# Optimization experiments

Measured on AMD Instinct MI355X. Metric: run time of the kernel, lower is better.

## Reference

```python
import jax, jax.numpy as jnp
import numpy as np

B, N, OBS, H, A = 1024, 64, 128, 256, 16
NH = 4
HD = H // NH


def _linear_params(key, fan_in, fan_out):
    k1, k2 = jax.random.split(key)
    bound = 1.0 / np.sqrt(fan_in)
    W = jax.random.uniform(k1, (fan_out, fan_in), jnp.float32, -bound, bound)
    b = jax.random.uniform(k2, (fan_out,), jnp.float32, -bound, bound)
    return W, b


def setup_inputs() -> dict:
    key = jax.random.key(0)
    ks = jax.random.split(key, 10)
    obs = jax.random.normal(ks[0], (B, N, OBS), jnp.float32)
    adj = jax.random.randint(ks[1], (B, N, N), 0, 2).astype(jnp.float32)
    # guarantee every row has at least one neighbor (self-loop) so softmax is finite
    adj = jnp.maximum(adj, jnp.eye(N, dtype=jnp.float32)[None])
    W1, b1 = _linear_params(ks[2], OBS, H)
    W2, b2 = _linear_params(ks[3], H, H)
    Wq, bq = _linear_params(ks[4], H, H)
    Wk, bk = _linear_params(ks[5], H, H)
    Wv, bv = _linear_params(ks[6], H, H)
    Wo, bo = _linear_params(ks[7], H, H)
    Wc, bc = _linear_params(ks[8], H, H)
    W3, b3 = _linear_params(ks[9], H, A)
    return dict(obs=obs, adj=adj, W1=W1, b1=b1, W2=W2, b2=b2,
                Wq=Wq, bq=bq, Wk=Wk, bk=bk, Wv=Wv, bv=bv,
                Wo=Wo, bo=bo, Wc=Wc, bc=bc, W3=W3, b3=b3)


def reference(obs, adj, W1, b1, W2, b2, Wq, bq, Wk, bk, Wv, bv, Wo, bo, Wc, bc, W3, b3):
    lin = lambda x, W, b: jnp.einsum('bnd,od->bno', x, W) + b
    x = jax.nn.relu(lin(obs, W1, b1))
    x = jax.nn.relu(lin(x, W2, b2))
    # multi-head attention with adjacency mask
    def heads(t):  # [B,N,H] -> [B,NH,N,HD]
        return t.reshape(B, N, NH, HD).transpose(0, 2, 1, 3)
    q = heads(lin(x, Wq, bq))
    k = heads(lin(x, Wk, bk))
    v = heads(lin(x, Wv, bv))
    scores = jnp.einsum('bhqd,bhkd->bhqk', q, k) / np.sqrt(HD).astype(np.float32)
    scores = jnp.where(adj[:, None] == 0, -jnp.inf, scores)
    attn = jax.nn.softmax(scores, axis=-1)
    out = jnp.einsum('bhqk,bhkd->bhqd', attn, v)
    out = out.transpose(0, 2, 1, 3).reshape(B, N, H)
    x = lin(out, Wo, bo)
    # communication: adj @ fc(x)
    x = jnp.einsum('bnm,bmh->bnh', adj, lin(x, Wc, bc))
    return lin(x, W3, b3)
```

## Files before the change

### kernel.cpp

```cpp
#include <hip/hip_runtime.h>
#include <stdint.h>

typedef unsigned short u16;
typedef unsigned long long u64;
typedef __attribute__((ext_vector_type(8))) short short8;
typedef __attribute__((ext_vector_type(4))) float f32x4;

#define MFMA16 __builtin_amdgcn_mfma_f32_16x16x32_bf16

#define B_ 1024
#define N_ 64
#define MTOT (B_ * N_)

__device__ __forceinline__ u16 f2bf(float f) {
  union { float f; uint32_t u; } v; v.f = f;
  uint32_t r = v.u + 0x7FFFu + ((v.u >> 16) & 1u);
  return (u16)(r >> 16);
}

union U8 { short8 v; u16 u[8]; };
union U4 { u64 v; u16 u[4]; };

__device__ __forceinline__ void cp16(const void* g, void* l) {
  __builtin_amdgcn_global_load_lds(
      (const __attribute__((address_space(1))) void*)g,
      (__attribute__((address_space(3))) void*)l, 16, 0, 0);
}

__global__ __launch_bounds__(256) void k_l1(
    const float* __restrict__ obs, u16* __restrict__ obsb,
    const float* __restrict__ Wc, const float* __restrict__ Wo,
    const float* __restrict__ bo, const float* __restrict__ bc,
    float* __restrict__ M1, float* __restrict__ bv,
    const float* __restrict__ W1, const float* __restrict__ W2,
    const float* __restrict__ Wq, const float* __restrict__ Wk,
    u16* o1, u16* o2, u16* oq, u16* ok) {
  const int bid = blockIdx.x, tid = threadIdx.x;
  if (bid < 4096) {
    const int e = (bid * 256 + tid) * 8;
    f32x4 a = *(const f32x4*)(obs + e);
    f32x4 b = *(const f32x4*)(obs + e + 4);
    U8 pk;
#pragma unroll
    for (int j = 0; j < 4; j++) { pk.u[j] = f2bf(a[j]); pk.u[4 + j] = f2bf(b[j]); }
    *(short8*)(obsb + e) = pk.v;
  } else if (bid < 4352) {
    __shared__ float wcr[256];
    __shared__ float red[4];
    const int j = bid - 4096, d = tid;
    wcr[d] = Wc[j * 256 + d];
    __syncthreads();
    float acc = 0.f;
    for (int i = 0; i < 256; i++) acc += wcr[i] * Wo[i * 256 + d];
    M1[j * 256 + d] = acc;
    float p = wcr[d] * bo[d];
    for (int off = 32; off >= 1; off >>= 1) p += __shfl_xor(p, off);
    if ((d & 63) == 0) red[d >> 6] = p;
    __syncthreads();
    if (d == 0) bv[j] = bc[j] + red[0] + red[1] + red[2] + red[3];
  } else {
    int off8 = (bid - 4352) * 256 + tid;
    const float* src; u16* dst;
    if      (off8 <  4096) { src = W1; dst = o1; }
    else if (off8 < 12288) { src = W2; dst = o2; off8 -= 4096; }
    else if (off8 < 20480) { src = Wq; dst = oq; off8 -= 12288; }
    else                   { src = Wk; dst = ok; off8 -= 20480; }
    const int e = off8 * 8;
    f32x4 a = *(const f32x4*)(src + e);
    f32x4 b = *(const f32x4*)(src + e + 4);
    U8 pk;
#pragma unroll
    for (int j = 0; j < 4; j++) { pk.u[j] = f2bf(a[j]); pk.u[4 + j] = f2bf(b[j]); }
    *(short8*)(dst + e) = pk.v;
  }
}

template<int K>
__device__ __forceinline__ void gemm_full(
    const u16* __restrict__ A, const u16* __restrict__ W,
    const float* __restrict__ bias, u16* __restrict__ C,
    const int m0, const bool relu, char* smem) {
  char* As  = smem;
  char* Bs0 = smem + 16384;
  char* Bs1 = smem + 32768;
  const int tid = threadIdx.x;
  const int lane = tid & 63, wid = tid >> 6;
  const int wr = wid >> 1, wc = wid & 1;
  const int ro = lane & 15, hi = lane >> 4;

  f32x4 acc0[4][4], acc1[4][4];
#pragma unroll
  for (int m = 0; m < 4; m++)
#pragma unroll
    for (int n = 0; n < 4; n++) {
      acc0[m][n] = (f32x4){0.f, 0.f, 0.f, 0.f};
      acc1[m][n] = (f32x4){0.f, 0.f, 0.f, 0.f};
    }

  for (int k0 = 0; k0 < K; k0 += 64) {
#pragma unroll
    for (int i = 0; i < 4; i++) {
      const int boff = i * 4096 + wid * 1024;
      const int t = boff + lane * 16;
      const int row = t >> 7;
      const int cb = (t & 127) ^ ((row & 7) << 4);
      cp16(A + (size_t)(m0 + row) * K + k0 + (cb >> 1), As + boff);
      cp16(W + (size_t)row * K + k0 + (cb >> 1), Bs0 + boff);
      cp16(W + (size_t)(128 + row) * K + k0 + (cb >> 1), Bs1 + boff);
    }
    __syncthreads();
#pragma unroll
    for (int kk = 0; kk < 64; kk += 32) {
      short8 af[4], b0[4], b1[4];
#pragma unroll
      for (int m = 0; m < 4; m++) {
        const int row = wr * 64 + m * 16 + ro;
        af[m] = *(const short8*)(As + ((row * 128 + (kk + hi * 8) * 2) ^ ((row & 7) << 4)));
      }
#pragma unroll
      for (int n = 0; n < 4; n++) {
        const int row = wc * 64 + n * 16 + ro;
        const int off = (row * 128 + (kk + hi * 8) * 2) ^ ((row & 7) << 4);
        b0[n] = *(const short8*)(Bs0 + off);
        b1[n] = *(const short8*)(Bs1 + off);
      }
#pragma unroll
      for (int m = 0; m < 4; m++)
#pragma unroll
        for (int n = 0; n < 4; n++) {
          acc0[m][n] = MFMA16(af[m], b0[n], acc0[m][n], 0, 0, 0);
          acc1[m][n] = MFMA16(af[m], b1[n], acc1[m][n], 0, 0, 0);
        }
    }
    __syncthreads();
  }

  u16 (*Cs)[136] = (u16(*)[136])smem;
  auto ep = [&](f32x4 (&acc)[4][4], const int n0) {
#pragma unroll
    for (int half = 0; half < 2; half++) {
      if (wr == half) {
#pragma unroll
        for (int n = 0; n < 4; n++) {
          const int col = wc * 64 + n * 16 + ro;
          const float bb = bias[n0 + col];
#pragma unroll
          for (int m = 0; m < 4; m++)
#pragma unroll
            for (int j = 0; j < 4; j++) {
              float val = acc[m][n][j] + bb;
              if (relu) val = fmaxf(val, 0.f);
              Cs[m * 16 + hi * 4 + j][col] = f2bf(val);
            }
        }
      }
      __syncthreads();
      for (int i = tid; i < 64 * 16; i += 256) {
        const int r = i >> 4, c = (i & 15) << 3;
        *(short8*)(C + (size_t)(m0 + half * 64 + r) * 256 + n0 + c) = *(short8*)&Cs[r][c];
      }
      __syncthreads();
    }
  };
  ep(acc0, 0);
  ep(acc1, 128);
}

__global__ __launch_bounds__(256, 2) void k_gemm1_prep2(
    const u16* __restrict__ obsb, const u16* __restrict__ W1b,
    const float* __restrict__ b1, u16* __restrict__ x1,
    const float* __restrict__ W3, const float* __restrict__ M1,
    const float* __restrict__ bvchain, const float* __restrict__ bvw,
    float* __restrict__ Wzf, float* __restrict__ bz) {
  __shared__ char smem[49152];
  if (blockIdx.x < 512) {
    gemm_full<128>(obsb, W1b, b1, x1, (int)blockIdx.x * 128, true, smem);
    return;
  }
  float* w3r = (float*)smem;
  float* red = (float*)(smem + 1024);
  const int a = blockIdx.x - 512, d = threadIdx.x;
  w3r[d] = W3[a * 256 + d];
  __syncthreads();
  float acc = 0.f;
  for (int j = 0; j < 256; j++) acc += w3r[j] * M1[j * 256 + d];
  Wzf[a * 256 + d] = acc;
  float p = w3r[d] * bvchain[d] + acc * bvw[d];
  for (int off = 32; off >= 1; off >>= 1) p += __shfl_xor(p, off);
  if ((d & 63) == 0) red[d >> 6] = p;
  __syncthreads();
  if (d == 0) bz[a] = red[0] + red[1] + red[2] + red[3];
}

__global__ __launch_bounds__(256, 2) void k_x2_prep3(
    const u16* __restrict__ x1, const u16* __restrict__ W2b,
    const float* __restrict__ b2, u16* __restrict__ x2,
    const float* __restrict__ Wzf, const float* __restrict__ Wv,
    u16* __restrict__ G) {
  __shared__ char smem[49152];
  if (blockIdx.x < 512) {
    gemm_full<256>(x1, W2b, b2, x2, (int)blockIdx.x * 128, true, smem);
    return;
  }
  const int g = blockIdx.x - 512, d2 = threadIdx.x;
  const int h = g >> 4, a = g & 15;
  float* wzr = (float*)smem;
  if (d2 < 64) wzr[d2] = Wzf[a * 256 + h * 64 + d2];
  __syncthreads();
  float acc = 0.f;
#pragma unroll 8
  for (int d = 0; d < 64; d++) acc += wzr[d] * Wv[(size_t)(h * 64 + d) * 256 + d2];
  G[g * 256 + d2] = f2bf(acc);
}

__global__ __launch_bounds__(256, 2) void k_qk_gemmv(
    const u16* __restrict__ x2,
    const u16* __restrict__ Wqb, const float* __restrict__ bq, u16* __restrict__ Qg,
    const u16* __restrict__ Wkb, const float* __restrict__ bk, u16* __restrict__ Kg,
    const u16* __restrict__ G, u16* __restrict__ Vzt) {
  __shared__ char smem[49152];
  const int bid = blockIdx.x;
  if (bid < 1024) {
    const int q = bid >> 4, r = bid & 15;
    const int mt = q * 8 + (r & 7);
    const int sub = r >> 3;
    gemm_full<256>(x2, sub ? Wkb : Wqb, sub ? bk : bq, sub ? Kg : Qg,
                   mt * 128, false, smem);
    return;
  }
  char* As = smem;
  char* Bs = smem + 16384;
  const int tid = threadIdx.x;
  const int lane = tid & 63, w = tid >> 6;
  const int ro = lane & 15, hi = lane >> 4;
  const int m0 = (bid - 1024) * 128;

  f32x4 acc[2][4];
#pragma unroll
  for (int m = 0; m < 2; m++)
#pragma unroll
    for (int n = 0; n < 4; n++) acc[m][n] = (f32x4){0.f, 0.f, 0.f, 0.f};

  for (int k0 = 0; k0 < 256; k0 += 64) {
#pragma unroll
    for (int i = 0; i < 4; i++) {
      const int boff = i * 4096 + w * 1024;
      const int t = boff + lane * 16;
      const int row = t >> 7;
      const int cb = (t & 127) ^ ((row & 7) << 4);
      cp16(x2 + (size_t)(m0 + row) * 256 + k0 + (cb >> 1), As + boff);
    }
    {
      const int boff = w * 1024;
      const int t = boff + lane * 16;
      const int row = t >> 7;
      const int cb = (t & 127) ^ ((row & 7) << 4);
      cp16(G + (size_t)row * 256 + k0 + (cb >> 1), Bs + boff);
      const int boff2 = 4096 + w * 1024;
      const int t2 = boff2 + lane * 16;
      const int row2 = t2 >> 7;
      const int cb2 = (t2 & 127) ^ ((row2 & 7) << 4);
      cp16(G + (size_t)row2 * 256 + k0 + (cb2 >> 1), Bs + boff2);
    }
    __syncthreads();
#pragma unroll
    for (int kk = 0; kk < 64; kk += 32) {
      short8 af[2], bfr[4];
#pragma unroll
      for (int m = 0; m < 2; m++) {
        const int row = w * 32 + m * 16 + ro;
        af[m] = *(const short8*)(As + ((row * 128 + (kk + hi * 8) * 2) ^ ((row & 7) << 4)));
      }
#pragma unroll
      for (int n = 0; n < 4; n++) {
        const int row = n * 16 + ro;
        bfr[n] = *(const short8*)(Bs + ((row * 128 + (kk + hi * 8) * 2) ^ ((row & 7) << 4)));
      }
#pragma unroll
      for (int m = 0; m < 2; m++)
#pragma unroll
        for (int n = 0; n < 4; n++)
          acc[m][n] = MFMA16(af[m], bfr[n], acc[m][n], 0, 0, 0);
    }
    __syncthreads();
  }

#pragma unroll
  for (int m = 0; m < 2; m++) {
    const int rbase = w * 32 + m * 16;
    const int bidx = (m0 >> 6) + (rbase >> 6);
    const int ke = (rbase + hi * 4) & 63;
#pragma unroll
    for (int n = 0; n < 4; n++) {
      const int c = n * 16 + ro;
      U4 pk;
#pragma unroll
      for (int j = 0; j < 4; j++) pk.u[j] = f2bf(acc[m][n][j]);
      *(u64*)(Vzt + (size_t)bidx * 4096 + (size_t)c * 64 + ke) = pk.v;
    }
  }
}

__global__ __launch_bounds__(256, 2) void attn_fused(
    const u16* __restrict__ Qg, const u16* __restrict__ Kg,
    const u16* __restrict__ Vzt, const float* __restrict__ adj,
    const float* __restrict__ bz, const float* __restrict__ b3,
    float* __restrict__ out) {
  __shared__ u16 Ps[4][64][72];
  __shared__ float Zs[4][64][16];
  __shared__ u64 adjm[64];
  __shared__ u16 chunk[64][4];

  const int b = blockIdx.x, tid = threadIdx.x;
  const int lane = tid & 63, w = tid >> 6;
  const int ro = lane & 15, hi = lane >> 4;
  const int hc = w * 64;
  const size_t base = (size_t)b * 64 * 256;

  short8 kb[4][2];
#pragma unroll
  for (int n = 0; n < 4; n++)
#pragma unroll
    for (int ks = 0; ks < 2; ks++)
      kb[n][ks] = *(const short8*)(Kg + base + (size_t)(n * 16 + ro) * 256 + hc + ks * 32 + hi * 8);

  {
    const int q = tid >> 2, qa = tid & 3;
    const float* ar = adj + ((size_t)b * 64 + q) * 64 + qa * 16;
    f32x4 a0 = *(const f32x4*)(ar);
    f32x4 a1 = *(const f32x4*)(ar + 4);
    f32x4 a2 = *(const f32x4*)(ar + 8);
    f32x4 a3 = *(const f32x4*)(ar + 12);
    unsigned m16 = 0;
#pragma unroll
    for (int i = 0; i < 4; i++) {
      m16 |= (unsigned)(a0[i] != 0.f) << i;
      m16 |= (unsigned)(a1[i] != 0.f) << (4 + i);
      m16 |= (unsigned)(a2[i] != 0.f) << (8 + i);
      m16 |= (unsigned)(a3[i] != 0.f) << (12 + i);
    }
    chunk[q][qa] = (u16)m16;
  }

  f32x4 s[4][4];
#pragma unroll
  for (int m = 0; m < 4; m++) {
    short8 af[2];
#pragma unroll
    for (int ks = 0; ks < 2; ks++)
      af[ks] = *(const short8*)(Qg + base + (size_t)(m * 16 + ro) * 256 + hc + ks * 32 + hi * 8);
#pragma unroll
    for (int n = 0; n < 4; n++) s[m][n] = (f32x4){0.f, 0.f, 0.f, 0.f};
#pragma unroll
    for (int ks = 0; ks < 2; ks++)
#pragma unroll
      for (int n = 0; n < 4; n++)
        s[m][n] = MFMA16(af[ks], kb[n][ks], s[m][n], 0, 0, 0);
  }

  short8 vz[2];
#pragma unroll
  for (int ks = 0; ks < 2; ks++)
    vz[ks] = *(const short8*)(Vzt + (size_t)b * 4096 + (size_t)(hc / 4 + ro) * 64 + ks * 32 + hi * 8);

  __syncthreads();
  if (tid < 64)
    adjm[tid] = (u64)chunk[tid][0] | ((u64)chunk[tid][1] << 16) |
                ((u64)chunk[tid][2] << 32) | ((u64)chunk[tid][3] << 48);
  __syncthreads();

#pragma unroll
  for (int m = 0; m < 4; m++) {
#pragma unroll
    for (int j = 0; j < 4; j++) {
      const int q = m * 16 + hi * 4 + j;
      const u64 msk = adjm[q];
      float sv[4], ev[4];
      float mx = -3.0e38f;
#pragma unroll
      for (int n = 0; n < 4; n++) {
        const bool on = (msk >> (n * 16 + ro)) & 1ull;
        sv[n] = on ? s[m][n][j] * 0.125f : -3.0e38f;
        mx = fmaxf(mx, sv[n]);
      }
      mx = fmaxf(mx, __shfl_xor(mx, 1));
      mx = fmaxf(mx, __shfl_xor(mx, 2));
      mx = fmaxf(mx, __shfl_xor(mx, 4));
      mx = fmaxf(mx, __shfl_xor(mx, 8));
      float sum = 0.f;
#pragma unroll
      for (int n = 0; n < 4; n++) {
        ev[n] = (sv[n] > -1.0e37f) ? __expf(sv[n] - mx) : 0.f;
        sum += ev[n];
      }
      sum += __shfl_xor(sum, 1);
      sum += __shfl_xor(sum, 2);
      sum += __shfl_xor(sum, 4);
      sum += __shfl_xor(sum, 8);
      const float inv = 1.0f / sum;
#pragma unroll
      for (int n = 0; n < 4; n++)
        Ps[w][q][n * 16 + ro] = f2bf(ev[n] * inv);
    }
  }

#pragma unroll
  for (int m = 0; m < 4; m++) {
    short8 pa[2];
    pa[0] = *(const short8*)&Ps[w][m * 16 + ro][hi * 8];
    pa[1] = *(const short8*)&Ps[w][m * 16 + ro][32 + hi * 8];
    f32x4 oz = (f32x4){0.f, 0.f, 0.f, 0.f};
#pragma unroll
    for (int ks = 0; ks < 2; ks++)
      oz = MFMA16(pa[ks], vz[ks], oz, 0, 0, 0);
#pragma unroll
    for (int j = 0; j < 4; j++)
      Zs[w][m * 16 + hi * 4 + j][ro] = oz[j];
  }
  __syncthreads();

  for (int i = tid; i < 1024; i += 256) {
    const int r = i >> 4, a = i & 15;
    Zs[0][r][a] += Zs[1][r][a] + Zs[2][r][a] + Zs[3][r][a];
  }
  __syncthreads();

  {
    const int n = tid >> 2, a4 = (tid & 3) << 2;
    const u64 msk = adjm[n];
    const float deg = (float)__popcll(msk);
    float a0 = 0.f, a1 = 0.f, a2 = 0.f, a3 = 0.f;
#pragma unroll 8
    for (int m = 0; m < 64; m++) {
      const float wv = (float)((msk >> m) & 1ull);
      f32x4 z = *(const f32x4*)&Zs[0][m][a4];
      a0 += wv * z[0]; a1 += wv * z[1]; a2 += wv * z[2]; a3 += wv * z[3];
    }
    f32x4 r;
    r[0] = a0 + b3[a4 + 0] + deg * bz[a4 + 0];
    r[1] = a1 + b3[a4 + 1] + deg * bz[a4 + 1];
    r[2] = a2 + b3[a4 + 2] + deg * bz[a4 + 2];
    r[3] = a3 + b3[a4 + 3] + deg * bz[a4 + 3];
    *(f32x4*)(out + ((size_t)b * 64 + n) * 16 + a4) = r;
  }
}

extern "C" void kernel_launch(void* const* d_in, const int* in_sizes, int n_in,
                              void* d_out, int out_size, void* d_ws, size_t ws_size,
                              hipStream_t stream) {
  const float* obs = (const float*)d_in[0];
  const float* adj = (const float*)d_in[1];
  const float* W1  = (const float*)d_in[2];
  const float* b1  = (const float*)d_in[3];
  const float* W2  = (const float*)d_in[4];
  const float* b2  = (const float*)d_in[5];
  const float* Wq  = (const float*)d_in[6];
  const float* bq  = (const float*)d_in[7];
  const float* Wk  = (const float*)d_in[8];
  const float* bk  = (const float*)d_in[9];
  const float* Wv  = (const float*)d_in[10];
  const float* bvw = (const float*)d_in[11];
  const float* Wo  = (const float*)d_in[12];
  const float* bo  = (const float*)d_in[13];
  const float* Wc  = (const float*)d_in[14];
  const float* bc  = (const float*)d_in[15];
  const float* W3  = (const float*)d_in[16];
  const float* b3  = (const float*)d_in[17];
  float* out = (float*)d_out;

  char* ws = (char*)d_ws;
  const size_t BIG = (size_t)MTOT * 256 * 2;
  u16* buf0 = (u16*)(ws);
  u16* buf1 = (u16*)(ws + BIG);
  u16* buf2 = (u16*)(ws + 2 * BIG);
  u16* buf3 = (u16*)(ws + 3 * BIG);
  char* p = ws + 4 * BIG;
  u16* W1b = (u16*)p;              p += 128 * 256 * 2;
  u16* W2b = (u16*)p;              p += 256 * 256 * 2;
  u16* Wqb = (u16*)p;              p += 256 * 256 * 2;
  u16* Wkb = (u16*)p;              p += 256 * 256 * 2;
  float* M1 = (float*)p;           p += 256 * 256 * 4;
  float* Wzf = (float*)p;          p += 16 * 256 * 4;
  u16* G   = (u16*)p;              p += 64 * 256 * 2;
  float* bv = (float*)p;           p += 256 * 4;
  float* bz = (float*)p;           p += 16 * 4;
  u16* obsb = (u16*)p;             p += (size_t)MTOT * 128 * 2;

  dim3 blk(256);
  k_l1<<<dim3(4464), blk, 0, stream>>>(obs, obsb, Wc, Wo, bo, bc, M1, bv,
                                       W1, W2, Wq, Wk, W1b, W2b, Wqb, Wkb);
  k_gemm1_prep2<<<dim3(528), blk, 0, stream>>>(obsb, W1b, b1, buf0,
                                               W3, M1, bv, bvw, Wzf, bz);
  k_x2_prep3<<<dim3(576), blk, 0, stream>>>(buf0, W2b, b2, buf1, Wzf, Wv, G);
  k_qk_gemmv<<<dim3(1536), blk, 0, stream>>>(buf1, Wqb, bq, buf2,
                                             Wkb, bk, buf3, G, buf0);
  attn_fused<<<dim3(1024), blk, 0, stream>>>(buf2, buf3, buf0, adj, bz, b3, out);
}
```

Baseline: 125.2 us.

## Double-buffer GEMM K-loop and fuse obs bf16 conversion into first GEMM

```diff
diff --git a/kernel.cpp b/kernel.cpp
--- a/kernel.cpp
+++ b/kernel.cpp
@@ -8,9 +8,7 @@
 
 #define MFMA16 __builtin_amdgcn_mfma_f32_16x16x32_bf16
 
-#define B_ 1024
-#define N_ 64
-#define MTOT (B_ * N_)
+#define MTOT 65536
 
 __device__ __forceinline__ u16 f2bf(float f) {
   union { float f; uint32_t u; } v; v.f = f;
@@ -28,7 +26,6 @@
 }
 
 __global__ __launch_bounds__(256) void k_l1(
-    const float* __restrict__ obs, u16* __restrict__ obsb,
     const float* __restrict__ Wc, const float* __restrict__ Wo,
     const float* __restrict__ bo, const float* __restrict__ bc,
     float* __restrict__ M1, float* __restrict__ bv,
@@ -36,18 +33,10 @@
     const float* __restrict__ Wq, const float* __restrict__ Wk,
     u16* o1, u16* o2, u16* oq, u16* ok) {
   const int bid = blockIdx.x, tid = threadIdx.x;
-  if (bid < 4096) {
-    const int e = (bid * 256 + tid) * 8;
-    f32x4 a = *(const f32x4*)(obs + e);
-    f32x4 b = *(const f32x4*)(obs + e + 4);
-    U8 pk;
-#pragma unroll
-    for (int j = 0; j < 4; j++) { pk.u[j] = f2bf(a[j]); pk.u[4 + j] = f2bf(b[j]); }
-    *(short8*)(obsb + e) = pk.v;
-  } else if (bid < 4352) {
+  if (bid < 256) {
     __shared__ float wcr[256];
     __shared__ float red[4];
-    const int j = bid - 4096, d = tid;
+    const int j = bid, d = tid;
     wcr[d] = Wc[j * 256 + d];
     __syncthreads();
     float acc = 0.f;
@@ -59,7 +48,7 @@
     __syncthreads();
     if (d == 0) bv[j] = bc[j] + red[0] + red[1] + red[2] + red[3];
   } else {
-    int off8 = (bid - 4352) * 256 + tid;
+    int off8 = (bid - 256) * 256 + tid;
     const float* src; u16* dst;
     if      (off8 <  4096) { src = W1; dst = o1; }
     else if (off8 < 12288) { src = W2; dst = o2; off8 -= 4096; }
@@ -75,14 +64,11 @@
   }
 }
 
-template<int K>
-__device__ __forceinline__ void gemm_full(
-    const u16* __restrict__ A, const u16* __restrict__ W,
+template<int K, bool AF32>
+__device__ __forceinline__ void gemm_full2(
+    const void* __restrict__ Ain, const u16* __restrict__ W,
     const float* __restrict__ bias, u16* __restrict__ C,
     const int m0, const bool relu, char* smem) {
-  char* As  = smem;
-  char* Bs0 = smem + 16384;
-  char* Bs1 = smem + 32768;
   const int tid = threadIdx.x;
   const int lane = tid & 63, wid = tid >> 6;
   const int wr = wid >> 1, wc = wid & 1;
@@ -97,43 +83,81 @@
       acc1[m][n] = (f32x4){0.f, 0.f, 0.f, 0.f};
     }
 
-  for (int k0 = 0; k0 < K; k0 += 64) {
+  auto stage = [&](int buf, int k0) {
+    char* Ax = smem + buf * 24576;
+    char* Bx = Ax + 8192;
+    if (AF32) {
+      const float* Af = (const float*)Ain;
+#pragma unroll
+      for (int it = 0; it < 2; it++) {
+        const int e = (tid + it * 256) * 8;
+        const int r = e >> 5, c = e & 31;
+        const float* s = Af + (size_t)(m0 + r) * K + k0 + c;
+        f32x4 a = *(const f32x4*)s, b = *(const f32x4*)(s + 4);
+        U8 pk;
+#pragma unroll
+        for (int j = 0; j < 4; j++) { pk.u[j] = f2bf(a[j]); pk.u[4 + j] = f2bf(b[j]); }
+        *(short8*)(Ax + ((r * 64 + c * 2) ^ ((r & 3) << 4))) = pk.v;
+      }
+    } else {
+      const u16* Ab = (const u16*)Ain;
+#pragma unroll
+      for (int i = 0; i < 2; i++) {
+        const int boff = i * 4096 + wid * 1024;
+        const int t = boff + lane * 16;
+        const int row = t >> 6;
+        const int cb = (t & 63) ^ ((row & 3) << 4);
+        cp16(Ab + (size_t)(m0 + row) * K + k0 + (cb >> 1), Ax + boff);
+      }
+    }
 #pragma unroll
     for (int i = 0; i < 4; i++) {
       const int boff = i * 4096 + wid * 1024;
       const int t = boff + lane * 16;
-      const int row = t >> 7;
-      const int cb = (t & 127) ^ ((row & 7) << 4);
-      cp16(A + (size_t)(m0 + row) * K + k0 + (cb >> 1), As + boff);
-      cp16(W + (size_t)row * K + k0 + (cb >> 1), Bs0 + boff);
-      cp16(W + (size_t)(128 + row) * K + k0 + (cb >> 1), Bs1 + boff);
-    }
+      const int row = t >> 6;
+      const int cb = (t & 63) ^ ((row & 3) << 4);
+      cp16(W + (size_t)row * K + k0 + (cb >> 1), Bx + boff);
+    }
+  };
+
+  auto compute = [&](int buf) {
+    char* Ax = smem + buf * 24576;
+    char* Bx = Ax + 8192;
+    short8 af[4], fb0[4], fb1[4];
+#pragma unroll
+    for (int m = 0; m < 4; m++) {
+      const int row = wr * 64 + m * 16 + ro;
+      af[m] = *(const short8*)(Ax + ((row * 64 + hi * 16) ^ ((row & 3) << 4)));
+    }
+#pragma unroll
+    for (int n = 0; n < 4; n++) {
+      const int r0 = wc * 64 + n * 16 + ro;
+      fb0[n] = *(const short8*)(Bx + ((r0 * 64 + hi * 16) ^ ((r0 & 3) << 4)));
+      const int r1 = 128 + r0;
+      fb1[n] = *(const short8*)(Bx + ((r1 * 64 + hi * 16) ^ ((r1 & 3) << 4)));
+    }
+    __builtin_amdgcn_s_setprio(1);
+#pragma unroll
+    for (int m = 0; m < 4; m++)
+#pragma unroll
+      for (int n = 0; n < 4; n++) {
+        acc0[m][n] = MFMA16(af[m], fb0[n], acc0[m][n], 0, 0, 0);
+        acc1[m][n] = MFMA16(af[m], fb1[n], acc1[m][n], 0, 0, 0);
+      }
+    __builtin_amdgcn_s_setprio(0);
+  };
+
+  stage(0, 0);
+  __syncthreads();
+  int cur = 0;
+  for (int k0 = 32; k0 < K; k0 += 32) {
+    stage(cur ^ 1, k0);
+    compute(cur);
     __syncthreads();
-#pragma unroll
-    for (int kk = 0; kk < 64; kk += 32) {
-      short8 af[4], b0[4], b1[4];
-#pragma unroll
-      for (int m = 0; m < 4; m++) {
-        const int row = wr * 64 + m * 16 + ro;
-        af[m] = *(const short8*)(As + ((row * 128 + (kk + hi * 8) * 2) ^ ((row & 7) << 4)));
-      }
-#pragma unroll
-      for (int n = 0; n < 4; n++) {
-        const int row = wc * 64 + n * 16 + ro;
-        const int off = (row * 128 + (kk + hi * 8) * 2) ^ ((row & 7) << 4);
-        b0[n] = *(const short8*)(Bs0 + off);
-        b1[n] = *(const short8*)(Bs1 + off);
-      }
-#pragma unroll
-      for (int m = 0; m < 4; m++)
-#pragma unroll
-        for (int n = 0; n < 4; n++) {
-          acc0[m][n] = MFMA16(af[m], b0[n], acc0[m][n], 0, 0, 0);
-          acc1[m][n] = MFMA16(af[m], b1[n], acc1[m][n], 0, 0, 0);
-        }
-    }
-    __syncthreads();
-  }
+    cur ^= 1;
+  }
+  compute(cur);
+  __syncthreads();
 
   u16 (*Cs)[136] = (u16(*)[136])smem;
   auto ep = [&](f32x4 (&acc)[4][4], const int n0) {
@@ -167,14 +191,14 @@
 }
 
 __global__ __launch_bounds__(256, 2) void k_gemm1_prep2(
-    const u16* __restrict__ obsb, const u16* __restrict__ W1b,
+    const float* __restrict__ obs, const u16* __restrict__ W1b,
     const float* __restrict__ b1, u16* __restrict__ x1,
     const float* __restrict__ W3, const float* __restrict__ M1,
     const float* __restrict__ bvchain, const float* __restrict__ bvw,
     float* __restrict__ Wzf, float* __restrict__ bz) {
   __shared__ char smem[49152];
   if (blockIdx.x < 512) {
-    gemm_full<128>(obsb, W1b, b1, x1, (int)blockIdx.x * 128, true, smem);
+    gemm_full2<128, true>(obs, W1b, b1, x1, (int)blockIdx.x * 128, true, smem);
     return;
   }
   float* w3r = (float*)smem;
@@ -199,7 +223,7 @@
     u16* __restrict__ G) {
   __shared__ char smem[49152];
   if (blockIdx.x < 512) {
-    gemm_full<256>(x1, W2b, b2, x2, (int)blockIdx.x * 128, true, smem);
+    gemm_full2<256, false>(x1, W2b, b2, x2, (int)blockIdx.x * 128, true, smem);
     return;
   }
   const int g = blockIdx.x - 512, d2 = threadIdx.x;
@@ -224,12 +248,10 @@
     const int q = bid >> 4, r = bid & 15;
     const int mt = q * 8 + (r & 7);
     const int sub = r >> 3;
-    gemm_full<256>(x2, sub ? Wkb : Wqb, sub ? bk : bq, sub ? Kg : Qg,
-                   mt * 128, false, smem);
+    gemm_full2<256, false>(x2, sub ? Wkb : Wqb, sub ? bk : bq, sub ? Kg : Qg,
+                           mt * 128, false, smem);
     return;
   }
-  char* As = smem;
-  char* Bs = smem + 16384;
   const int tid = threadIdx.x;
   const int lane = tid & 63, w = tid >> 6;
   const int ro = lane & 15, hi = lane >> 4;
@@ -241,49 +263,58 @@
 #pragma unroll
     for (int n = 0; n < 4; n++) acc[m][n] = (f32x4){0.f, 0.f, 0.f, 0.f};
 
-  for (int k0 = 0; k0 < 256; k0 += 64) {
-#pragma unroll
-    for (int i = 0; i < 4; i++) {
+  auto stage = [&](int buf, int k0) {
+    char* Ax = smem + buf * 12288;
+    char* Bx = Ax + 8192;
+#pragma unroll
+    for (int i = 0; i < 2; i++) {
       const int boff = i * 4096 + w * 1024;
       const int t = boff + lane * 16;
-      const int row = t >> 7;
-      const int cb = (t & 127) ^ ((row & 7) << 4);
-      cp16(x2 + (size_t)(m0 + row) * 256 + k0 + (cb >> 1), As + boff);
+      const int row = t >> 6;
+      const int cb = (t & 63) ^ ((row & 3) << 4);
+      cp16(x2 + (size_t)(m0 + row) * 256 + k0 + (cb >> 1), Ax + boff);
     }
     {
       const int boff = w * 1024;
       const int t = boff + lane * 16;
-      const int row = t >> 7;
-      const int cb = (t & 127) ^ ((row & 7) << 4);
-      cp16(G + (size_t)row * 256 + k0 + (cb >> 1), Bs + boff);
-      const int boff2 = 4096 + w * 1024;
-      const int t2 = boff2 + lane * 16;
-      const int row2 = t2 >> 7;
-      const int cb2 = (t2 & 127) ^ ((row2 & 7) << 4);
-      cp16(G + (size_t)row2 * 256 + k0 + (cb2 >> 1), Bs + boff2);
-    }
+      const int row = t >> 6;
+      const int cb = (t & 63) ^ ((row & 3) << 4);
+      cp16(G + (size_t)row * 256 + k0 + (cb >> 1), Bx + boff);
+    }
+  };
+  auto compute = [&](int buf) {
+    char* Ax = smem + buf * 12288;
+    char* Bx = Ax + 8192;
+    short8 af[2], fb[4];
+#pragma unroll
+    for (int m = 0; m < 2; m++) {
+      const int row = w * 32 + m * 16 + ro;
+      af[m] = *(const short8*)(Ax + ((row * 64 + hi * 16) ^ ((row & 3) << 4)));
+    }
+#pragma unroll
+    for (int n = 0; n < 4; n++) {
+      const int row = n * 16 + ro;
+      fb[n] = *(const short8*)(Bx + ((row * 64 + hi * 16) ^ ((row & 3) << 4)));
+    }
+    __builtin_amdgcn_s_setprio(1);
+#pragma unroll
+    for (int m = 0; m < 2; m++)
+#pragma unroll
+      for (int n = 0; n < 4; n++)
+        acc[m][n] = MFMA16(af[m], fb[n], acc[m][n], 0, 0, 0);
+    __builtin_amdgcn_s_setprio(0);
+  };
+
+  stage(0, 0);
+  __syncthreads();
+  int cur = 0;
+  for (int k0 = 32; k0 < 256; k0 += 32) {
+    stage(cur ^ 1, k0);
+    compute(cur);
     __syncthreads();
-#pragma unroll
-    for (int kk = 0; kk < 64; kk += 32) {
-      short8 af[2], bfr[4];
-#pragma unroll
-      for (int m = 0; m < 2; m++) {
-        const int row = w * 32 + m * 16 + ro;
-        af[m] = *(const short8*)(As + ((row * 128 + (kk + hi * 8) * 2) ^ ((row & 7) << 4)));
-      }
-#pragma unroll
-      for (int n = 0; n < 4; n++) {
-        const int row = n * 16 + ro;
-        bfr[n] = *(const short8*)(Bs + ((row * 128 + (kk + hi * 8) * 2) ^ ((row & 7) << 4)));
-      }
-#pragma unroll
-      for (int m = 0; m < 2; m++)
-#pragma unroll
-        for (int n = 0; n < 4; n++)
-          acc[m][n] = MFMA16(af[m], bfr[n], acc[m][n], 0, 0, 0);
-    }
-    __syncthreads();
-  }
+    cur ^= 1;
+  }
+  compute(cur);
 
 #pragma unroll
   for (int m = 0; m < 2; m++) {
@@ -484,12 +515,11 @@
   u16* G   = (u16*)p;              p += 64 * 256 * 2;
   float* bv = (float*)p;           p += 256 * 4;
   float* bz = (float*)p;           p += 16 * 4;
-  u16* obsb = (u16*)p;             p += (size_t)MTOT * 128 * 2;
 
   dim3 blk(256);
-  k_l1<<<dim3(4464), blk, 0, stream>>>(obs, obsb, Wc, Wo, bo, bc, M1, bv,
-                                       W1, W2, Wq, Wk, W1b, W2b, Wqb, Wkb);
-  k_gemm1_prep2<<<dim3(528), blk, 0, stream>>>(obsb, W1b, b1, buf0,
+  k_l1<<<dim3(368), blk, 0, stream>>>(Wc, Wo, bo, bc, M1, bv,
+                                      W1, W2, Wq, Wk, W1b, W2b, Wqb, Wkb);
+  k_gemm1_prep2<<<dim3(528), blk, 0, stream>>>(obs, W1b, b1, buf0,
                                                W3, M1, bv, bvw, Wzf, bz);
   k_x2_prep3<<<dim3(576), blk, 0, stream>>>(buf0, W2b, b2, buf1, Wzf, Wv, G);
   k_qk_gemmv<<<dim3(1536), blk, 0, stream>>>(buf1, Wqb, bq, buf2,
```

Result: faster. 122.5 us (-2.2%).
